# Performance work log

Hardware: AMD Instinct MI355X
Metric: run time of the kernel (lower is better)

## Reference

```python
import jax, jax.numpy as jnp
import numpy as np

B, T, E = 2, 4096, 1024
H = 16
D = E // H  # head_len = 64


def setup_inputs() -> dict:
    key = jax.random.key(0)
    ks = jax.random.split(key, 6)
    s = 1.0 / np.sqrt(E)
    return {
        "x": jax.random.normal(ks[0], (B, T, E), dtype=jnp.float32),
        # torch nn.Linear weights: shape (out, in), y = x @ W.T
        "Wq": jax.random.uniform(ks[1], (E, E), jnp.float32, -s, s),
        "Wk": jax.random.uniform(ks[2], (E, E), jnp.float32, -s, s),
        "Wv": jax.random.uniform(ks[3], (E, E), jnp.float32, -s, s),
        "Wo": jax.random.uniform(ks[4], (E, E), jnp.float32, -s, s),
        "bo": jax.random.uniform(ks[5], (E,), jnp.float32, -s, s),
    }


def reference(x, Wq, Wk, Wv, Wo, bo):
    Bx, Tx, Ex = x.shape
    q = x @ Wq.T
    k = x @ Wk.T
    v = x @ Wv.T
    # (B, T, H, D) -> (B, H, T, D)
    q = q.reshape(Bx, Tx, H, D).transpose(0, 2, 1, 3)
    k = k.reshape(Bx, Tx, H, D).transpose(0, 2, 1, 3)
    v = v.reshape(Bx, Tx, H, D).transpose(0, 2, 1, 3)
    # scores: (B, H, T, T), scaled by sqrt(head_len)
    sim = jnp.einsum("bhqd,bhkd->bhqk", q, k) / jnp.sqrt(jnp.float32(D))
    causal = jnp.tril(jnp.ones((Tx, Tx), dtype=bool))  # True = keep
    sim = jnp.where(causal[None, None], sim, -jnp.inf)
    attn = jax.nn.softmax(sim, axis=-1)
    # dropout_rate = 0.0 (eval) -> identity
    out = jnp.einsum("bhqk,bhkd->bhqd", attn, v)
    out = out.transpose(0, 2, 1, 3).reshape(Bx, Tx, Ex)
    return out @ Wo.T + bo
```

## Files before the change

kernel.cpp:

```cpp
#include <hip/hip_runtime.h>

typedef unsigned short bf16_t;
typedef __bf16 bf16x8 __attribute__((ext_vector_type(8)));
typedef float  v4f   __attribute__((ext_vector_type(4)));

__device__ __forceinline__ bf16_t f2bf(float f) {
    union { float f; unsigned u; } a; a.f = f;
    unsigned r = a.u + 0x7FFFu + ((a.u >> 16) & 1u);
    return (bf16_t)(r >> 16);
}
__device__ __forceinline__ unsigned fbits(float f) {
    union { float f; unsigned u; } a; a.f = f; return a.u;
}
__device__ __forceinline__ unsigned pk_trunc(float lo, float hi) {
    return (fbits(lo) >> 16) | (fbits(hi) & 0xFFFF0000u);
}

#define GL16(g, l) __builtin_amdgcn_global_load_lds( \
    (__attribute__((address_space(1))) void*)(g),    \
    (__attribute__((address_space(3))) void*)(l), 16, 0, 0)

#define QSCALE 0.18033688011f

__global__ __launch_bounds__(256) void cvt_all(
    const float4* __restrict__ x,  const float4* __restrict__ wq,
    const float4* __restrict__ wk, const float4* __restrict__ wv,
    const float4* __restrict__ wo,
    ushort4* __restrict__ xb, ushort4* __restrict__ wqkv, ushort4* __restrict__ wob) {
    int i = blockIdx.x * 256 + threadIdx.x;
    const float4* s; ushort4* d; int off;
    if (i < 2097152) { s = x; d = xb; off = i; }
    else {
        int wdx = (i - 2097152) >> 18;
        off = (i - 2097152) & 262143;
        if      (wdx == 0) { s = wq; d = wqkv; }
        else if (wdx == 1) { s = wk; d = wqkv + 262144; }
        else if (wdx == 2) { s = wv; d = wqkv + 524288; }
        else               { s = wo; d = wob; }
    }
    float4 v = s[off];
    ushort4 o;
    o.x = f2bf(v.x); o.y = f2bf(v.y); o.z = f2bf(v.z); o.w = f2bf(v.w);
    d[off] = o;
}

#define GEMM_MAINLOOP(A_, W_)                                                          \
    __shared__ bf16_t SMEM[8192];                                                      \
    bf16_t* As = SMEM; bf16_t* Bs = SMEM + 4096;                                       \
    const int tid = threadIdx.x;                                                       \
    const int w = tid >> 6, lane = tid & 63;                                           \
    const int lrow = lane & 15, lq = lane >> 4;                                        \
    const int m0 = blockIdx.y * 128, n0 = blockIdx.x * 128;                            \
    const int srow = w * 16 + (lane >> 2);                                             \
    const int sk = (lane & 3) * 8;                                                     \
    const int wm = (w & 1) * 64, wn = (w >> 1) * 64;                                   \
    v4f acc[4][4];                                                                     \
    _Pragma("unroll") for (int i = 0; i < 4; ++i)                                      \
        _Pragma("unroll") for (int j = 0; j < 4; ++j)                                  \
            acc[i][j] = (v4f){0.f, 0.f, 0.f, 0.f};                                     \
    for (int k0 = 0; k0 < 1024; k0 += 32) {                                            \
        __syncthreads();                                                               \
        GL16(A_ + (size_t)(m0 + srow) * 1024 + k0 + sk,      (char*)As + w * 1024);    \
        GL16(A_ + (size_t)(m0 + 64 + srow) * 1024 + k0 + sk, (char*)As + 4096 + w * 1024); \
        GL16(W_ + (size_t)(n0 + srow) * 1024 + k0 + sk,      (char*)Bs + w * 1024);    \
        GL16(W_ + (size_t)(n0 + 64 + srow) * 1024 + k0 + sk, (char*)Bs + 4096 + w * 1024); \
        __syncthreads();                                                               \
        bf16x8 af[4], bf[4];                                                           \
        _Pragma("unroll") for (int i = 0; i < 4; ++i)                                  \
            af[i] = *(const bf16x8*)&As[(wm + i * 16 + lrow) * 32 + lq * 8];           \
        _Pragma("unroll") for (int j = 0; j < 4; ++j)                                  \
            bf[j] = *(const bf16x8*)&Bs[(wn + j * 16 + lrow) * 32 + lq * 8];           \
        _Pragma("unroll") for (int i = 0; i < 4; ++i)                                  \
            _Pragma("unroll") for (int j = 0; j < 4; ++j)                              \
                acc[i][j] = __builtin_amdgcn_mfma_f32_16x16x32_bf16(af[i], bf[j],      \
                                                                    acc[i][j], 0, 0, 0); \
    }

__global__ __launch_bounds__(256) void gemm_qkv_kernel(
    const bf16_t* __restrict__ A, const bf16_t* __restrict__ W,
    bf16_t* __restrict__ Qb, bf16_t* __restrict__ Kb, bf16_t* __restrict__ Vtb) {
    GEMM_MAINLOOP(A, W)
    const int x = blockIdx.x;
    const int b = m0 >> 12, t0 = m0 & 4095;
    if (x < 8) {
#pragma unroll
        for (int i = 0; i < 4; ++i)
#pragma unroll
            for (int j = 0; j < 4; ++j)
#pragma unroll
                for (int r = 0; r < 4; ++r) {
                    int t = t0 + wm + i * 16 + lq * 4 + r;
                    int n = n0 + wn + j * 16 + lrow;
                    int h = n >> 6, d = n & 63;
                    Qb[(((size_t)b * 16 + h) * 4096 + t) * 64 + d] =
                        f2bf(acc[i][j][r] * QSCALE);
                }
    } else if (x < 16) {
#pragma unroll
        for (int i = 0; i < 4; ++i)
#pragma unroll
            for (int j = 0; j < 4; ++j)
#pragma unroll
                for (int r = 0; r < 4; ++r) {
                    int t = t0 + wm + i * 16 + lq * 4 + r;
                    int nn = n0 + wn + j * 16 + lrow - 1024;
                    int h = nn >> 6, d = nn & 63;
                    Kb[(((size_t)b * 16 + h) * 4096 + t) * 64 + d] = f2bf(acc[i][j][r]);
                }
    } else {
        const int d0 = n0 - 2048;
#pragma unroll 1
        for (int p = 0; p < 2; ++p) {
            __syncthreads();
            if ((w >> 1) == p) {
#pragma unroll
                for (int i = 0; i < 4; ++i)
#pragma unroll
                    for (int j = 0; j < 4; ++j) {
                        int row = j * 16 + lrow;
                        int swz = (row & 7) << 1;
                        int g = (wm >> 2) + i * 4 + lq;
                        uint2 u;
                        u.x = (unsigned)f2bf(acc[i][j][0]) | ((unsigned)f2bf(acc[i][j][1]) << 16);
                        u.y = (unsigned)f2bf(acc[i][j][2]) | ((unsigned)f2bf(acc[i][j][3]) << 16);
                        *(uint2*)&SMEM[row * 128 + ((g ^ swz) << 2)] = u;
                    }
            }
            __syncthreads();
#pragma unroll
            for (int uu = 0; uu < 4; ++uu) {
                int unit = tid + 256 * uu;
                int row = unit >> 4, seg = unit & 15;
                uint4 val = *(const uint4*)&SMEM[row * 128 + ((seg ^ (row & 7)) << 3)];
                *(uint4*)&Vtb[((size_t)b * 1024 + d0 + p * 64 + row) * 4096 + t0 + seg * 8] = val;
            }
        }
    }
}

__global__ __launch_bounds__(256) void gemm_out_kernel(
    const bf16_t* __restrict__ A, const bf16_t* __restrict__ W,
    const float* __restrict__ bo, float* __restrict__ out) {
    GEMM_MAINLOOP(A, W)
#pragma unroll
    for (int j = 0; j < 4; ++j) {
        int n = n0 + wn + j * 16 + lrow;
        float bias = bo[n];
#pragma unroll
        for (int i = 0; i < 4; ++i)
#pragma unroll
            for (int r = 0; r < 4; ++r) {
                int m = m0 + wm + i * 16 + lq * 4 + r;
                out[(size_t)m * 1024 + n] = acc[i][j][r] + bias;
            }
    }
}

__global__ __launch_bounds__(256, 2) void attn_kernel(
    const bf16_t* __restrict__ Q, const bf16_t* __restrict__ K,
    const bf16_t* __restrict__ Vt, bf16_t* __restrict__ O) {
    __shared__ bf16_t Kls[2][2][64 * 32];
    __shared__ bf16_t Vls[2][2][64 * 32];
    __shared__ bf16_t Plds[4][32 * 64];
    const int tid = threadIdx.x;
    const int w = tid >> 6, lane = tid & 63;
    const int lrow = lane & 15, lq = lane >> 4;
    const int bh = blockIdx.y;
    const int g = blockIdx.x;

    const bf16_t* Qh = Q + (size_t)bh * (4096 * 64);
    const bf16_t* Kh = K + (size_t)bh * (4096 * 64);
    const bf16_t* Vh = Vt + (size_t)bh * (64 * 4096);
    bf16_t* Pw = Plds[w];
    const int b = bh >> 4, h = bh & 15;

    const int srow = lane >> 2;
    const int soff = (((lane & 3) ^ (srow & 3))) * 8;
    const int kswz = (lq ^ (lrow & 3)) * 8;
    const int pswz = (lrow & 7) << 1;

    bf16x8 ones;
#pragma unroll
    for (int i = 0; i < 8; ++i) ones[i] = (__bf16)1.0f;

#pragma unroll 1
    for (int mem = 0; mem < 2; ++mem) {
        const int j = mem ? (31 - g) : g;
        const int q0 = j * 128;
        const int q0w = q0 + w * 32;
        const int nt = 2 * j + 2;
        const int wlast = 2 * j + (w >> 1);

        bf16x8 qf[2][2];
#pragma unroll
        for (int sub = 0; sub < 2; ++sub)
#pragma unroll
            for (int dk = 0; dk < 2; ++dk)
                qf[sub][dk] = *(const bf16x8*)&Qh[(size_t)(q0w + sub * 16 + lrow) * 64 + dk * 32 + lq * 8];

        v4f oacc[2][4];
        v4f lacc[2];
#pragma unroll
        for (int s2 = 0; s2 < 2; ++s2) {
            lacc[s2] = (v4f){0.f, 0.f, 0.f, 0.f};
#pragma unroll
            for (int d = 0; d < 4; ++d) oacc[s2][d] = (v4f){0.f, 0.f, 0.f, 0.f};
        }

        auto stage = [&](int kt, int buf) {
            const int kc0 = kt << 6;
#pragma unroll
            for (int i = 0; i < 2; ++i) {
                int idx = w * 2 + i;
                int half = idx >> 2, rg = idx & 3;
                GL16(Kh + (size_t)(kc0 + rg * 16 + srow) * 64 + half * 32 + soff,
                     (char*)&Kls[buf][half][rg * 512]);
                GL16(Vh + (size_t)(rg * 16 + srow) * 4096 + kc0 + half * 32 + soff,
                     (char*)&Vls[buf][half][rg * 512]);
            }
        };

        stage(0, 0);
        for (int kt = 0; kt < nt; ++kt) {
            const int buf = kt & 1;
            __syncthreads();
            if (kt + 1 < nt) stage(kt + 1, buf ^ 1);
            if (kt > wlast) continue;
            const int kc0 = kt << 6;
            const bool diag = (kt == wlast);

            bf16x8 kf0[4], kf1[4];
#pragma unroll
            for (int c = 0; c < 4; ++c) {
                kf0[c] = *(const bf16x8*)&Kls[buf][0][(c * 16 + lrow) * 32 + kswz];
                kf1[c] = *(const bf16x8*)&Kls[buf][1][(c * 16 + lrow) * 32 + kswz];
            }
            bf16x8 vf[4][2];
#pragma unroll
            for (int d = 0; d < 4; ++d)
#pragma unroll
                for (int kh = 0; kh < 2; ++kh)
                    vf[d][kh] = *(const bf16x8*)&Vls[buf][kh][(d * 16 + lrow) * 32 + kswz];

#pragma unroll
            for (int sub = 0; sub < 2; ++sub) {
                const int qrow = sub * 16 + lrow;
                const int qglob = q0w + qrow;

                v4f st[4];
#pragma unroll
                for (int c = 0; c < 4; ++c) {
                    v4f t0v = (v4f){0.f, 0.f, 0.f, 0.f};
                    t0v = __builtin_amdgcn_mfma_f32_16x16x32_bf16(kf0[c], qf[sub][0], t0v, 0, 0, 0);
                    st[c] = __builtin_amdgcn_mfma_f32_16x16x32_bf16(kf1[c], qf[sub][1], t0v, 0, 0, 0);
                }

#pragma unroll
                for (int c = 0; c < 4; ++c) {
                    float p[4];
#pragma unroll
                    for (int r = 0; r < 4; ++r) {
                        float pv = __builtin_amdgcn_exp2f(st[c][r]);
                        if (diag) {
                            int tg = kc0 + c * 16 + lq * 4 + r;
                            pv = (tg > qglob) ? 0.f : pv;
                        }
                        p[r] = pv;
                    }
                    uint2 u;
                    u.x = pk_trunc(p[0], p[1]);
                    u.y = pk_trunc(p[2], p[3]);
                    *(uint2*)&Pw[qrow * 64 + (((c * 4 + lq) ^ pswz) << 2)] = u;
                }

                bf16x8 pf[2];
#pragma unroll
                for (int kh = 0; kh < 2; ++kh) {
                    int s0 = kh * 8 + lq * 2;
                    pf[kh] = *(const bf16x8*)&Pw[qrow * 64 + ((s0 ^ pswz) << 2)];
                }

#pragma unroll
                for (int kh = 0; kh < 2; ++kh) {
                    lacc[sub] = __builtin_amdgcn_mfma_f32_16x16x32_bf16(pf[kh], ones, lacc[sub], 0, 0, 0);
#pragma unroll
                    for (int d = 0; d < 4; ++d)
                        oacc[sub][d] = __builtin_amdgcn_mfma_f32_16x16x32_bf16(pf[kh], vf[d][kh], oacc[sub][d], 0, 0, 0);
                }
            }
        }

#pragma unroll
        for (int sub = 0; sub < 2; ++sub) {
            float rl[4];
#pragma unroll
            for (int r = 0; r < 4; ++r) rl[r] = 1.0f / lacc[sub][r];
#pragma unroll
            for (int d = 0; d < 4; ++d)
#pragma unroll
                for (int r = 0; r < 4; ++r) {
                    int t = q0w + sub * 16 + lq * 4 + r;
                    O[((size_t)b * 4096 + t) * 1024 + h * 64 + d * 16 + lrow] =
                        f2bf(oacc[sub][d][r] * rl[r]);
                }
        }
    }
}

extern "C" void kernel_launch(void* const* d_in, const int* in_sizes, int n_in,
                              void* d_out, int out_size, void* d_ws, size_t ws_size,
                              hipStream_t stream) {
    const float* x  = (const float*)d_in[0];
    const float* Wq = (const float*)d_in[1];
    const float* Wk = (const float*)d_in[2];
    const float* Wv = (const float*)d_in[3];
    const float* Wo = (const float*)d_in[4];
    const float* bo = (const float*)d_in[5];
    float* out = (float*)d_out;

    char* ws = (char*)d_ws;
    bf16_t* xb   = (bf16_t*)(ws + 0);
    bf16_t* Wqkv = (bf16_t*)(ws + 16777216);
    bf16_t* Wob  = (bf16_t*)(ws + 23068672);
    bf16_t* Qb   = (bf16_t*)(ws + 25165824);
    bf16_t* Kb   = (bf16_t*)(ws + 41943040);
    bf16_t* Vtb  = (bf16_t*)(ws + 58720256);
    bf16_t* Ob   = (bf16_t*)(ws + 75497472);

    cvt_all<<<12288, 256, 0, stream>>>((const float4*)x, (const float4*)Wq,
                                       (const float4*)Wk, (const float4*)Wv,
                                       (const float4*)Wo,
                                       (ushort4*)xb, (ushort4*)Wqkv, (ushort4*)Wob);

    gemm_qkv_kernel<<<dim3(24, 64), 256, 0, stream>>>(xb, Wqkv, Qb, Kb, Vtb);

    attn_kernel<<<dim3(16, 32), 256, 0, stream>>>(Qb, Kb, Vtb, Ob);

    gemm_out_kernel<<<dim3(8, 64), 256, 0, stream>>>(Ob, Wob, bo, out);
}
```

Baseline: 316.0 us.

## Swizzle LDS tiles, swap GEMM operands for vector stores, split attention blocks

The GEMM main loop gains an XOR swizzle on the LDS tile to cut bank conflicts. The QKV and output GEMMs swap their A and B operands so each lane holds four contiguous outputs, which allows packed 8-byte and float4 stores; this also removes the LDS transpose staging for V. The attention kernel drops its paired-tile loop (one block per query tile, grid doubled, heaviest tiles first), uses a new K/V swizzle, and swaps the MFMA operands so the output is stored as packed vectors. The larger grid trades in-block load balancing for more blocks and relies on the hardware scheduler.

```diff
diff --git a/kernel.cpp b/kernel.cpp
--- a/kernel.cpp
+++ b/kernel.cpp
@@ -12,7 +12,10 @@
 __device__ __forceinline__ unsigned fbits(float f) {
     union { float f; unsigned u; } a; a.f = f; return a.u;
 }
-__device__ __forceinline__ unsigned pk_trunc(float lo, float hi) {
+__device__ __forceinline__ unsigned pk2(float lo, float hi) {
+    return (unsigned)f2bf(lo) | ((unsigned)f2bf(hi) << 16);
+}
+__device__ __forceinline__ unsigned pk2t(float lo, float hi) {
     return (fbits(lo) >> 16) | (fbits(hi) & 0xFFFF0000u);
 }
 
@@ -44,15 +47,15 @@
     d[off] = o;
 }
 
-#define GEMM_MAINLOOP(A_, W_)                                                          \
+#define GEMM_MAINLOOP(PA_, baseA_, PB_, baseB_)                                        \
     __shared__ bf16_t SMEM[8192];                                                      \
     bf16_t* As = SMEM; bf16_t* Bs = SMEM + 4096;                                       \
     const int tid = threadIdx.x;                                                       \
     const int w = tid >> 6, lane = tid & 63;                                           \
     const int lrow = lane & 15, lq = lane >> 4;                                        \
-    const int m0 = blockIdx.y * 128, n0 = blockIdx.x * 128;                            \
     const int srow = w * 16 + (lane >> 2);                                             \
-    const int sk = (lane & 3) * 8;                                                     \
+    const int sk = ((lane & 3) ^ ((lane >> 3) & 3)) * 8;                               \
+    const int rswz = (lq ^ ((lrow >> 1) & 3)) * 8;                                     \
     const int wm = (w & 1) * 64, wn = (w >> 1) * 64;                                   \
     v4f acc[4][4];                                                                     \
     _Pragma("unroll") for (int i = 0; i < 4; ++i)                                      \
@@ -60,16 +63,16 @@
             acc[i][j] = (v4f){0.f, 0.f, 0.f, 0.f};                                     \
     for (int k0 = 0; k0 < 1024; k0 += 32) {                                            \
         __syncthreads();                                                               \
-        GL16(A_ + (size_t)(m0 + srow) * 1024 + k0 + sk,      (char*)As + w * 1024);    \
-        GL16(A_ + (size_t)(m0 + 64 + srow) * 1024 + k0 + sk, (char*)As + 4096 + w * 1024); \
-        GL16(W_ + (size_t)(n0 + srow) * 1024 + k0 + sk,      (char*)Bs + w * 1024);    \
-        GL16(W_ + (size_t)(n0 + 64 + srow) * 1024 + k0 + sk, (char*)Bs + 4096 + w * 1024); \
+        GL16(PA_ + (size_t)(baseA_ + srow) * 1024 + k0 + sk,      (char*)As + w * 1024);    \
+        GL16(PA_ + (size_t)(baseA_ + 64 + srow) * 1024 + k0 + sk, (char*)As + 4096 + w * 1024); \
+        GL16(PB_ + (size_t)(baseB_ + srow) * 1024 + k0 + sk,      (char*)Bs + w * 1024);    \
+        GL16(PB_ + (size_t)(baseB_ + 64 + srow) * 1024 + k0 + sk, (char*)Bs + 4096 + w * 1024); \
         __syncthreads();                                                               \
         bf16x8 af[4], bf[4];                                                           \
         _Pragma("unroll") for (int i = 0; i < 4; ++i)                                  \
-            af[i] = *(const bf16x8*)&As[(wm + i * 16 + lrow) * 32 + lq * 8];           \
+            af[i] = *(const bf16x8*)&As[(wm + i * 16 + lrow) * 32 + rswz];             \
         _Pragma("unroll") for (int j = 0; j < 4; ++j)                                  \
-            bf[j] = *(const bf16x8*)&Bs[(wn + j * 16 + lrow) * 32 + lq * 8];           \
+            bf[j] = *(const bf16x8*)&Bs[(wn + j * 16 + lrow) * 32 + rswz];             \
         _Pragma("unroll") for (int i = 0; i < 4; ++i)                                  \
             _Pragma("unroll") for (int j = 0; j < 4; ++j)                              \
                 acc[i][j] = __builtin_amdgcn_mfma_f32_16x16x32_bf16(af[i], bf[j],      \
@@ -77,82 +80,67 @@
     }
 
 __global__ __launch_bounds__(256) void gemm_qkv_kernel(
-    const bf16_t* __restrict__ A, const bf16_t* __restrict__ W,
+    const bf16_t* __restrict__ xb, const bf16_t* __restrict__ Wqkv,
     bf16_t* __restrict__ Qb, bf16_t* __restrict__ Kb, bf16_t* __restrict__ Vtb) {
-    GEMM_MAINLOOP(A, W)
     const int x = blockIdx.x;
-    const int b = m0 >> 12, t0 = m0 & 4095;
-    if (x < 8) {
+    const int m0 = blockIdx.y * 128;
+    const bool isV = (x >= 16);
+    const bf16_t* PA = isV ? xb : Wqkv;
+    const bf16_t* PB = isV ? Wqkv : xb;
+    const int baseA = isV ? m0 : x * 128;
+    const int baseB = isV ? x * 128 : m0;
+    GEMM_MAINLOOP(PA, baseA, PB, baseB)
+    if (!isV) {
+        bf16_t* dst = (x < 8) ? Qb : Kb;
+        const float sc = (x < 8) ? QSCALE : 1.0f;
+        const int nb = (x < 8) ? x * 128 : x * 128 - 1024;
 #pragma unroll
         for (int i = 0; i < 4; ++i)
 #pragma unroll
-            for (int j = 0; j < 4; ++j)
-#pragma unroll
-                for (int r = 0; r < 4; ++r) {
-                    int t = t0 + wm + i * 16 + lq * 4 + r;
-                    int n = n0 + wn + j * 16 + lrow;
-                    int h = n >> 6, d = n & 63;
-                    Qb[(((size_t)b * 16 + h) * 4096 + t) * 64 + d] =
-                        f2bf(acc[i][j][r] * QSCALE);
-                }
-    } else if (x < 16) {
+            for (int j = 0; j < 4; ++j) {
+                int n = nb + wm + i * 16 + lq * 4;
+                int t = m0 + wn + j * 16 + lrow;
+                int bb = t >> 12, tt = t & 4095;
+                int hh = n >> 6, dd = n & 63;
+                uint2 u;
+                u.x = pk2(acc[i][j][0] * sc, acc[i][j][1] * sc);
+                u.y = pk2(acc[i][j][2] * sc, acc[i][j][3] * sc);
+                *(uint2*)&dst[(((size_t)bb * 16 + hh) * 4096 + tt) * 64 + dd] = u;
+            }
+    } else {
 #pragma unroll
         for (int i = 0; i < 4; ++i)
 #pragma unroll
-            for (int j = 0; j < 4; ++j)
-#pragma unroll
-                for (int r = 0; r < 4; ++r) {
-                    int t = t0 + wm + i * 16 + lq * 4 + r;
-                    int nn = n0 + wn + j * 16 + lrow - 1024;
-                    int h = nn >> 6, d = nn & 63;
-                    Kb[(((size_t)b * 16 + h) * 4096 + t) * 64 + d] = f2bf(acc[i][j][r]);
-                }
-    } else {
-        const int d0 = n0 - 2048;
-#pragma unroll 1
-        for (int p = 0; p < 2; ++p) {
-            __syncthreads();
-            if ((w >> 1) == p) {
-#pragma unroll
-                for (int i = 0; i < 4; ++i)
-#pragma unroll
-                    for (int j = 0; j < 4; ++j) {
-                        int row = j * 16 + lrow;
-                        int swz = (row & 7) << 1;
-                        int g = (wm >> 2) + i * 4 + lq;
-                        uint2 u;
-                        u.x = (unsigned)f2bf(acc[i][j][0]) | ((unsigned)f2bf(acc[i][j][1]) << 16);
-                        u.y = (unsigned)f2bf(acc[i][j][2]) | ((unsigned)f2bf(acc[i][j][3]) << 16);
-                        *(uint2*)&SMEM[row * 128 + ((g ^ swz) << 2)] = u;
-                    }
-            }
-            __syncthreads();
-#pragma unroll
-            for (int uu = 0; uu < 4; ++uu) {
-                int unit = tid + 256 * uu;
-                int row = unit >> 4, seg = unit & 15;
-                uint4 val = *(const uint4*)&SMEM[row * 128 + ((seg ^ (row & 7)) << 3)];
-                *(uint4*)&Vtb[((size_t)b * 1024 + d0 + p * 64 + row) * 4096 + t0 + seg * 8] = val;
-            }
-        }
+            for (int j = 0; j < 4; ++j) {
+                int t = m0 + wm + i * 16 + lq * 4;
+                int vr = x * 128 - 2048 + wn + j * 16 + lrow;
+                int bb = t >> 12, tt = t & 4095;
+                uint2 u;
+                u.x = pk2(acc[i][j][0], acc[i][j][1]);
+                u.y = pk2(acc[i][j][2], acc[i][j][3]);
+                *(uint2*)&Vtb[((size_t)bb * 1024 + vr) * 4096 + tt] = u;
+            }
     }
 }
 
 __global__ __launch_bounds__(256) void gemm_out_kernel(
-    const bf16_t* __restrict__ A, const bf16_t* __restrict__ W,
+    const bf16_t* __restrict__ Ob, const bf16_t* __restrict__ Wob,
     const float* __restrict__ bo, float* __restrict__ out) {
-    GEMM_MAINLOOP(A, W)
-#pragma unroll
-    for (int j = 0; j < 4; ++j) {
-        int n = n0 + wn + j * 16 + lrow;
-        float bias = bo[n];
-#pragma unroll
-        for (int i = 0; i < 4; ++i)
-#pragma unroll
-            for (int r = 0; r < 4; ++r) {
-                int m = m0 + wm + i * 16 + lq * 4 + r;
-                out[(size_t)m * 1024 + n] = acc[i][j][r] + bias;
-            }
+    const int x = blockIdx.x;
+    const int m0 = blockIdx.y * 128;
+    const int nA = x * 128;
+    GEMM_MAINLOOP(Wob, nA, Ob, m0)
+#pragma unroll
+    for (int i = 0; i < 4; ++i) {
+        int n = nA + wm + i * 16 + lq * 4;
+        float4 bv = *(const float4*)&bo[n];
+#pragma unroll
+        for (int j = 0; j < 4; ++j) {
+            int m = m0 + wn + j * 16 + lrow;
+            float4 o = {acc[i][j][0] + bv.x, acc[i][j][1] + bv.y,
+                        acc[i][j][2] + bv.z, acc[i][j][3] + bv.w};
+            *(float4*)&out[(size_t)m * 1024 + n] = o;
+        }
     }
 }
 
@@ -166,7 +154,11 @@
     const int w = tid >> 6, lane = tid & 63;
     const int lrow = lane & 15, lq = lane >> 4;
     const int bh = blockIdx.y;
-    const int g = blockIdx.x;
+    const int j = 31 - blockIdx.x;
+    const int q0 = j * 128;
+    const int q0w = q0 + w * 32;
+    const int nt = 2 * j + 2;
+    const int wlast = 2 * j + (w >> 1);
 
     const bf16_t* Qh = Q + (size_t)bh * (4096 * 64);
     const bf16_t* Kh = K + (size_t)bh * (4096 * 64);
@@ -175,134 +167,123 @@
     const int b = bh >> 4, h = bh & 15;
 
     const int srow = lane >> 2;
-    const int soff = (((lane & 3) ^ (srow & 3))) * 8;
-    const int kswz = (lq ^ (lrow & 3)) * 8;
+    const int soff = ((lane & 3) ^ ((srow >> 1) & 3)) * 8;
+    const int kswz = (lq ^ ((lrow >> 1) & 3)) * 8;
     const int pswz = (lrow & 7) << 1;
 
     bf16x8 ones;
 #pragma unroll
     for (int i = 0; i < 8; ++i) ones[i] = (__bf16)1.0f;
 
-#pragma unroll 1
-    for (int mem = 0; mem < 2; ++mem) {
-        const int j = mem ? (31 - g) : g;
-        const int q0 = j * 128;
-        const int q0w = q0 + w * 32;
-        const int nt = 2 * j + 2;
-        const int wlast = 2 * j + (w >> 1);
-
-        bf16x8 qf[2][2];
-#pragma unroll
-        for (int sub = 0; sub < 2; ++sub)
-#pragma unroll
-            for (int dk = 0; dk < 2; ++dk)
-                qf[sub][dk] = *(const bf16x8*)&Qh[(size_t)(q0w + sub * 16 + lrow) * 64 + dk * 32 + lq * 8];
-
-        v4f oacc[2][4];
-        v4f lacc[2];
-#pragma unroll
-        for (int s2 = 0; s2 < 2; ++s2) {
-            lacc[s2] = (v4f){0.f, 0.f, 0.f, 0.f};
-#pragma unroll
-            for (int d = 0; d < 4; ++d) oacc[s2][d] = (v4f){0.f, 0.f, 0.f, 0.f};
-        }
-
-        auto stage = [&](int kt, int buf) {
-            const int kc0 = kt << 6;
-#pragma unroll
-            for (int i = 0; i < 2; ++i) {
-                int idx = w * 2 + i;
-                int half = idx >> 2, rg = idx & 3;
-                GL16(Kh + (size_t)(kc0 + rg * 16 + srow) * 64 + half * 32 + soff,
-                     (char*)&Kls[buf][half][rg * 512]);
-                GL16(Vh + (size_t)(rg * 16 + srow) * 4096 + kc0 + half * 32 + soff,
-                     (char*)&Vls[buf][half][rg * 512]);
-            }
-        };
-
-        stage(0, 0);
-        for (int kt = 0; kt < nt; ++kt) {
-            const int buf = kt & 1;
-            __syncthreads();
-            if (kt + 1 < nt) stage(kt + 1, buf ^ 1);
-            if (kt > wlast) continue;
-            const int kc0 = kt << 6;
-            const bool diag = (kt == wlast);
-
-            bf16x8 kf0[4], kf1[4];
+    bf16x8 qf[2][2];
+#pragma unroll
+    for (int sub = 0; sub < 2; ++sub)
+#pragma unroll
+        for (int dk = 0; dk < 2; ++dk)
+            qf[sub][dk] = *(const bf16x8*)&Qh[(size_t)(q0w + sub * 16 + lrow) * 64 + dk * 32 + lq * 8];
+
+    v4f oacc[2][4];
+    v4f lacc[2];
+#pragma unroll
+    for (int s2 = 0; s2 < 2; ++s2) {
+        lacc[s2] = (v4f){0.f, 0.f, 0.f, 0.f};
+#pragma unroll
+        for (int d = 0; d < 4; ++d) oacc[s2][d] = (v4f){0.f, 0.f, 0.f, 0.f};
+    }
+
+    auto stage = [&](int kt, int buf) {
+        const size_t kc0 = (size_t)kt << 6;
+#pragma unroll
+        for (int i = 0; i < 2; ++i) {
+            int u = w * 2 + i;
+            int half = u >> 2, rg = u & 3;
+            GL16(Kh + (kc0 + rg * 16 + srow) * 64 + half * 32 + soff,
+                 (char*)&Kls[buf][half][rg * 512]);
+            GL16(Vh + (size_t)(rg * 16 + srow) * 4096 + kc0 + half * 32 + soff,
+                 (char*)&Vls[buf][half][rg * 512]);
+        }
+    };
+
+    stage(0, 0);
+    for (int kt = 0; kt < nt; ++kt) {
+        const int buf = kt & 1;
+        __syncthreads();
+        if (kt + 1 < nt) stage(kt + 1, buf ^ 1);
+        if (kt > wlast) continue;
+        const int kc0 = kt << 6;
+        const bool diag = (kt == wlast);
+
+        bf16x8 kf0[4], kf1[4];
+#pragma unroll
+        for (int c = 0; c < 4; ++c) {
+            kf0[c] = *(const bf16x8*)&Kls[buf][0][(c * 16 + lrow) * 32 + kswz];
+            kf1[c] = *(const bf16x8*)&Kls[buf][1][(c * 16 + lrow) * 32 + kswz];
+        }
+        bf16x8 vf[4][2];
+#pragma unroll
+        for (int d = 0; d < 4; ++d)
+#pragma unroll
+            for (int kh = 0; kh < 2; ++kh)
+                vf[d][kh] = *(const bf16x8*)&Vls[buf][kh][(d * 16 + lrow) * 32 + kswz];
+
+#pragma unroll
+        for (int sub = 0; sub < 2; ++sub) {
+            const int qrow = sub * 16 + lrow;
+            const int qglob = q0w + qrow;
+
+            v4f st[4];
 #pragma unroll
             for (int c = 0; c < 4; ++c) {
-                kf0[c] = *(const bf16x8*)&Kls[buf][0][(c * 16 + lrow) * 32 + kswz];
-                kf1[c] = *(const bf16x8*)&Kls[buf][1][(c * 16 + lrow) * 32 + kswz];
-            }
-            bf16x8 vf[4][2];
-#pragma unroll
-            for (int d = 0; d < 4; ++d)
-#pragma unroll
-                for (int kh = 0; kh < 2; ++kh)
-                    vf[d][kh] = *(const bf16x8*)&Vls[buf][kh][(d * 16 + lrow) * 32 + kswz];
-
-#pragma unroll
-            for (int sub = 0; sub < 2; ++sub) {
-                const int qrow = sub * 16 + lrow;
-                const int qglob = q0w + qrow;
-
-                v4f st[4];
-#pragma unroll
-                for (int c = 0; c < 4; ++c) {
-                    v4f t0v = (v4f){0.f, 0.f, 0.f, 0.f};
-                    t0v = __builtin_amdgcn_mfma_f32_16x16x32_bf16(kf0[c], qf[sub][0], t0v, 0, 0, 0);
-                    st[c] = __builtin_amdgcn_mfma_f32_16x16x32_bf16(kf1[c], qf[sub][1], t0v, 0, 0, 0);
+                v4f t0v = (v4f){0.f, 0.f, 0.f, 0.f};
+                t0v = __builtin_amdgcn_mfma_f32_16x16x32_bf16(kf0[c], qf[sub][0], t0v, 0, 0, 0);
+                st[c] = __builtin_amdgcn_mfma_f32_16x16x32_bf16(kf1[c], qf[sub][1], t0v, 0, 0, 0);
+            }
+
+#pragma unroll
+            for (int c = 0; c < 4; ++c) {
+                float p[4];
+#pragma unroll
+                for (int r = 0; r < 4; ++r) {
+                    float pv = __builtin_amdgcn_exp2f(st[c][r]);
+                    if (diag) {
+                        int tg = kc0 + c * 16 + lq * 4 + r;
+                        pv = (tg > qglob) ? 0.f : pv;
+                    }
+                    p[r] = pv;
                 }
-
-#pragma unroll
-                for (int c = 0; c < 4; ++c) {
-                    float p[4];
-#pragma unroll
-                    for (int r = 0; r < 4; ++r) {
-                        float pv = __builtin_amdgcn_exp2f(st[c][r]);
-                        if (diag) {
-                            int tg = kc0 + c * 16 + lq * 4 + r;
-                            pv = (tg > qglob) ? 0.f : pv;
-                        }
-                        p[r] = pv;
-                    }
-                    uint2 u;
-                    u.x = pk_trunc(p[0], p[1]);
-                    u.y = pk_trunc(p[2], p[3]);
-                    *(uint2*)&Pw[qrow * 64 + (((c * 4 + lq) ^ pswz) << 2)] = u;
-                }
-
-                bf16x8 pf[2];
-#pragma unroll
-                for (int kh = 0; kh < 2; ++kh) {
-                    int s0 = kh * 8 + lq * 2;
-                    pf[kh] = *(const bf16x8*)&Pw[qrow * 64 + ((s0 ^ pswz) << 2)];
-                }
-
-#pragma unroll
-                for (int kh = 0; kh < 2; ++kh) {
-                    lacc[sub] = __builtin_amdgcn_mfma_f32_16x16x32_bf16(pf[kh], ones, lacc[sub], 0, 0, 0);
-#pragma unroll
-                    for (int d = 0; d < 4; ++d)
-                        oacc[sub][d] = __builtin_amdgcn_mfma_f32_16x16x32_bf16(pf[kh], vf[d][kh], oacc[sub][d], 0, 0, 0);
-                }
-            }
-        }
-
-#pragma unroll
-        for (int sub = 0; sub < 2; ++sub) {
-            float rl[4];
-#pragma unroll
-            for (int r = 0; r < 4; ++r) rl[r] = 1.0f / lacc[sub][r];
-#pragma unroll
-            for (int d = 0; d < 4; ++d)
-#pragma unroll
-                for (int r = 0; r < 4; ++r) {
-                    int t = q0w + sub * 16 + lq * 4 + r;
-                    O[((size_t)b * 4096 + t) * 1024 + h * 64 + d * 16 + lrow] =
-                        f2bf(oacc[sub][d][r] * rl[r]);
-                }
+                uint2 u;
+                u.x = pk2t(p[0], p[1]);
+                u.y = pk2t(p[2], p[3]);
+                *(uint2*)&Pw[qrow * 64 + (((c * 4 + lq) ^ pswz) << 2)] = u;
+            }
+
+            bf16x8 pf[2];
+#pragma unroll
+            for (int kh = 0; kh < 2; ++kh) {
+                int s0 = kh * 8 + lq * 2;
+                pf[kh] = *(const bf16x8*)&Pw[qrow * 64 + ((s0 ^ pswz) << 2)];
+            }
+
+#pragma unroll
+            for (int kh = 0; kh < 2; ++kh) {
+                lacc[sub] = __builtin_amdgcn_mfma_f32_16x16x32_bf16(ones, pf[kh], lacc[sub], 0, 0, 0);
+#pragma unroll
+                for (int d = 0; d < 4; ++d)
+                    oacc[sub][d] = __builtin_amdgcn_mfma_f32_16x16x32_bf16(vf[d][kh], pf[kh], oacc[sub][d], 0, 0, 0);
+            }
+        }
+    }
+
+#pragma unroll
+    for (int sub = 0; sub < 2; ++sub) {
+        float rl = 1.0f / lacc[sub][0];
+        size_t rowbase = ((size_t)b * 4096 + q0w + sub * 16 + lrow) * 1024 + h * 64 + lq * 4;
+#pragma unroll
+        for (int d = 0; d < 4; ++d) {
+            uint2 u;
+            u.x = pk2(oacc[sub][d][0] * rl, oacc[sub][d][1] * rl);
+            u.y = pk2(oacc[sub][d][2] * rl, oacc[sub][d][3] * rl);
+            *(uint2*)&O[rowbase + d * 16] = u;
         }
     }
 }
@@ -334,7 +315,7 @@
 
     gemm_qkv_kernel<<<dim3(24, 64), 256, 0, stream>>>(xb, Wqkv, Qb, Kb, Vtb);
 
-    attn_kernel<<<dim3(16, 32), 256, 0, stream>>>(Qb, Kb, Vtb, Ob);
+    attn_kernel<<<dim3(32, 32), 256, 0, stream>>>(Qb, Kb, Vtb, Ob);
 
     gemm_out_kernel<<<dim3(8, 64), 256, 0, stream>>>(Ob, Wob, bo, out);
 }
```

Measured after the change: 393.9 us. 24.6% more time.
